# Performance work log

Hardware: AMD Instinct MI355X
Metric: run time of the kernel (lower is better)

The kernel has to match this reference:

```python
import jax, jax.numpy as jnp
import numpy as np

N = 50000
E = 800000
IN_DIM = 128
OUT_DIM = 128
EDGE_DIM = 3
H = 4
HD = OUT_DIM // H  # 32
SCALE = HD ** -0.5


def setup_inputs() -> dict:
    key = jax.random.key(0)
    ks = jax.random.split(key, 10)
    x = jax.random.normal(ks[0], (N, IN_DIM), dtype=jnp.float32)
    edge_index = jax.random.randint(ks[1], (2, E), 0, N, dtype=jnp.int64)
    edge_attr = jax.random.normal(ks[2], (E, EDGE_DIM), dtype=jnp.float32)
    s = 1.0 / np.sqrt(IN_DIM)
    Wq = jax.random.normal(ks[3], (IN_DIM, H * HD), dtype=jnp.float32) * s
    Wk = jax.random.normal(ks[4], (IN_DIM, H * HD), dtype=jnp.float32) * s
    Wv = jax.random.normal(ks[5], (IN_DIM, H * HD), dtype=jnp.float32) * s
    We = jax.random.normal(ks[6], (EDGE_DIM, H), dtype=jnp.float32) * (1.0 / np.sqrt(EDGE_DIM))
    Wo = jax.random.normal(ks[7], (H * HD, OUT_DIM), dtype=jnp.float32) * (1.0 / np.sqrt(H * HD))
    bo = jnp.zeros((OUT_DIM,), dtype=jnp.float32)
    Wm = jax.random.normal(ks[8], (IN_DIM + OUT_DIM, OUT_DIM), dtype=jnp.float32) * (1.0 / np.sqrt(IN_DIM + OUT_DIM))
    bm = jnp.zeros((OUT_DIM,), dtype=jnp.float32)
    return {"x": x, "edge_index": edge_index, "edge_attr": edge_attr,
            "Wq": Wq, "Wk": Wk, "Wv": Wv, "We": We, "Wo": Wo, "bo": bo,
            "Wm": Wm, "bm": bm}


def reference(x, edge_index, edge_attr, Wq, Wk, Wv, We, Wo, bo, Wm, bm):
    n = x.shape[0]
    src = edge_index[0]
    dst = edge_index[1]
    Q = (x @ Wq).reshape(n, H, HD)
    K = (x @ Wk).reshape(n, H, HD)
    V = (x @ Wv).reshape(n, H, HD)
    edge_bias = edge_attr @ We                                  # [E, H]
    attn = jnp.sum(Q[dst] * K[src], axis=-1) * SCALE + edge_bias  # [E, H]
    attn = jnp.where(attn >= 0, attn, 0.2 * attn)               # leaky_relu(0.2)
    # NOTE: original uses a single GLOBAL max over all edges/heads for stability
    attn_exp = jnp.exp(attn - jnp.max(attn))
    attn_sum = jax.ops.segment_sum(attn_exp, dst, num_segments=n)  # [N, H]
    attn_norm = attn_exp / jnp.maximum(attn_sum[dst], 1e-12)
    # dropout disabled (eval mode)
    weighted_V = V[src] * attn_norm[:, :, None]                 # [E, H, HD]
    agg = jax.ops.segment_sum(weighted_V, dst, num_segments=n)  # [N, H, HD]
    agg = agg.reshape(n, H * HD) @ Wo + bo                      # [N, OUT]
    h = jnp.concatenate([x, agg], axis=1) @ Wm + bm
    return jax.nn.relu(h)
```

## Files before the change

kernel.cpp:

```cpp
#include <hip/hip_runtime.h>
#include <hip/hip_bf16.h>
#include <math.h>

#define NN 50000
#define NE 800000
#define DIM 128
#define NH 4
#define HD 32
#define ATTN_SCALE 0.17677669529663687f
#define MTILE 64
#define GEMM_BLOCKS 782
#define NBK 782
#define PTS 2048
#define HBLKS 104

#define K1_QKV_BASE 104
#define K1_WXB_BASE 296
#define K1_GRID     361
#define K3_PART_N     391
#define K3_PACKO_BASE 391
#define K3_XCVT_BASE  519
#define K3_GRID       6769
#define K4_CSR_N 782
#define K4_GRID  1564

typedef unsigned int uint;
typedef unsigned short ushort;
typedef __attribute__((ext_vector_type(8))) short short8;
typedef __attribute__((ext_vector_type(4))) float f32x4;

__device__ inline ushort f2bf(float f) {
    __hip_bfloat16 h = __float2bfloat16(f);
    return *(ushort*)&h;
}
__device__ inline float bflo(uint u) { return __uint_as_float(u << 16); }
__device__ inline float bfhi(uint u) { return __uint_as_float(u & 0xffff0000u); }

__global__ __launch_bounds__(256) void k1_kernel(
    const int* __restrict__ dst, int* __restrict__ bkt_cnt,
    const float* __restrict__ Wq, const float* __restrict__ Wk,
    const float* __restrict__ Wv, short* __restrict__ BpQKV,
    const float* __restrict__ Wo, const float* __restrict__ Wm,
    const float* __restrict__ bo, const float* __restrict__ bm,
    float* __restrict__ Wx, float* __restrict__ bprime)
{
    const int bid = blockIdx.x;
    const int tid = threadIdx.x;

    if (bid < HBLKS) {
        __shared__ int c[NBK];
        for (int l = tid; l < NBK; l += 256) c[l] = 0;
        __syncthreads();
        for (int e = bid * 256 + tid; e < NE; e += HBLKS * 256)
            atomicAdd(&c[dst[e] >> 6], 1);
        __syncthreads();
        for (int l = tid; l < NBK; l += 256)
            if (c[l]) atomicAdd(&bkt_cnt[l], c[l]);
    } else if (bid < K1_WXB_BASE) {
        const int idx = (bid - K1_QKV_BASE) * 256 + tid;
        const int j = idx & 7, lane = (idx >> 3) & 63;
        const int rest = idx >> 9;
        const int nt = rest % 24, kc = rest / 24;
        const int k = kc * 32 + (lane >> 4) * 8 + j;
        const int n = nt * 16 + (lane & 15);
        const float* W = (n < 128) ? Wq : (n < 256 ? Wk : Wv);
        BpQKV[idx] = (short)f2bf(W[k * 128 + (n & 127)]);
    } else {
        const int r = (bid - K1_WXB_BASE) * 2 + (tid >> 7);
        const int j = tid & 127;
        if (r < 128) {
            float acc = 0.f;
            for (int t = 0; t < 128; ++t)
                acc = fmaf(Wo[r * 128 + t], Wm[(128 + t) * 128 + j], acc);
            Wx[r * 128 + j] = acc;
        } else if (r == 128) {
            float acc = bm[j];
            for (int t = 0; t < 128; ++t)
                acc = fmaf(bo[t], Wm[(128 + t) * 128 + j], acc);
            bprime[j] = acc;
        }
    }
}

__global__ __launch_bounds__(256) void bkt_scan_kernel(
    const int* __restrict__ bkt_cnt,
    int* __restrict__ bkt_base, int* __restrict__ bkt_cursor,
    int* __restrict__ rowptr)
{
    __shared__ int part[256];
    const int tid = threadIdx.x;
    const int b0 = tid * 4;
    int v0 = 0, v1 = 0, v2 = 0, v3 = 0;
    if (b0 + 0 < NBK) v0 = bkt_cnt[b0 + 0];
    if (b0 + 1 < NBK) v1 = bkt_cnt[b0 + 1];
    if (b0 + 2 < NBK) v2 = bkt_cnt[b0 + 2];
    if (b0 + 3 < NBK) v3 = bkt_cnt[b0 + 3];
    const int s = v0 + v1 + v2 + v3;
    part[tid] = s;
    __syncthreads();
    for (int off = 1; off < 256; off <<= 1) {
        const int y = (tid >= off) ? part[tid - off] : 0;
        __syncthreads();
        part[tid] += y;
        __syncthreads();
    }
    const int ex = part[tid] - s;
    const int r0 = ex, r1 = ex + v0, r2 = ex + v0 + v1, r3 = ex + v0 + v1 + v2;
    if (b0 + 0 < NBK) { bkt_base[b0 + 0] = r0; bkt_cursor[b0 + 0] = r0; }
    if (b0 + 1 < NBK) { bkt_base[b0 + 1] = r1; bkt_cursor[b0 + 1] = r1; }
    if (b0 + 2 < NBK) { bkt_base[b0 + 2] = r2; bkt_cursor[b0 + 2] = r2; }
    if (b0 + 3 < NBK) { bkt_base[b0 + 3] = r3; bkt_cursor[b0 + 3] = r3; }
    if (tid == 255) bkt_base[NBK] = part[255];
    if (tid == 0)   rowptr[NN] = NE;
}

__global__ __launch_bounds__(256) void k3_kernel(
    const int* __restrict__ src, const int* __restrict__ dst,
    const float* __restrict__ edge_attr, const float* __restrict__ We,
    int* __restrict__ bkt_cursor,
    uint* __restrict__ ppack, uint2* __restrict__ pebp,
    const float* __restrict__ Wm, const float* __restrict__ Wx,
    short* __restrict__ BpOut,
    const float* __restrict__ x, ushort* __restrict__ xb)
{
    const int bid = blockIdx.x;
    const int tid = threadIdx.x;

    if (bid < K3_PART_N) {
        __shared__ int cnt[NBK], rbase[NBK], cnt2[NBK];
        for (int l = tid; l < NBK; l += 256) cnt[l] = 0;
        __syncthreads();
        const int e0 = bid * PTS;
        #pragma unroll
        for (int it = 0; it < 8; ++it) {
            const int e = e0 + it * 256 + tid;
            if (e < NE) atomicAdd(&cnt[dst[e] >> 6], 1);
        }
        __syncthreads();
        for (int l = tid; l < NBK; l += 256) {
            const int c = cnt[l];
            rbase[l] = c ? atomicAdd(&bkt_cursor[l], c) : 0;
            cnt2[l] = 0;
        }
        __syncthreads();
        #pragma unroll
        for (int it = 0; it < 8; ++it) {
            const int e = e0 + it * 256 + tid;
            if (e < NE) {
                const int d = dst[e];
                const int b = d >> 6;
                const int r = atomicAdd(&cnt2[b], 1);
                const int pos = rbase[b] + r;
                ppack[pos] = (uint)src[e] | ((uint)(d & 63) << 16);
                const float a0 = edge_attr[e * 3 + 0];
                const float a1 = edge_attr[e * 3 + 1];
                const float a2 = edge_attr[e * 3 + 2];
                const float b0 = a0 * We[0] + a1 * We[4] + a2 * We[8];
                const float b1 = a0 * We[1] + a1 * We[5] + a2 * We[9];
                const float b2 = a0 * We[2] + a1 * We[6] + a2 * We[10];
                const float b3 = a0 * We[3] + a1 * We[7] + a2 * We[11];
                uint2 ep;
                ep.x = (uint)f2bf(b0) | ((uint)f2bf(b1) << 16);
                ep.y = (uint)f2bf(b2) | ((uint)f2bf(b3) << 16);
                pebp[pos] = ep;
            }
        }
    } else if (bid < K3_XCVT_BASE) {
        const int idx = (bid - K3_PACKO_BASE) * 256 + tid;
        const int j = idx & 7, lane = (idx >> 3) & 63;
        const int rest = idx >> 9;
        const int nt = rest & 7, kc = rest >> 3;
        const int k = kc * 32 + (lane >> 4) * 8 + j;
        const int n = nt * 16 + (lane & 15);
        const float v = (k < 128) ? Wm[k * 128 + n] : Wx[(k - 128) * 128 + n];
        BpOut[idx] = (short)f2bf(v);
    } else {
        const int i = (bid - K3_XCVT_BASE) * 256 + tid;
        const float4 v = ((const float4*)x)[i];
        ushort4 o;
        o.x = f2bf(v.x); o.y = f2bf(v.y); o.z = f2bf(v.z); o.w = f2bf(v.w);
        ((ushort4*)xb)[i] = o;
    }
}

__global__ __launch_bounds__(256) void k4_kernel(
    const int* __restrict__ bkt_base,
    const uint* __restrict__ ppack, const uint2* __restrict__ pebp,
    int* __restrict__ rowptr, uint4* __restrict__ edata,
    const ushort* __restrict__ xb, const short* __restrict__ BpQKV,
    ushort* __restrict__ Qb, ushort* __restrict__ KVb)
{
    const int bid = blockIdx.x;
    const int tid = threadIdx.x;

    if (bid < K4_CSR_N) {
        __shared__ int cnt[64];
        __shared__ int pre[64];
        const int base = bkt_base[bid];
        const int n = bkt_base[bid + 1] - base;
        const int node0 = bid << 6;

        if (tid < 64) cnt[tid] = 0;
        __syncthreads();
        for (int i = base + tid; i < base + n; i += 256)
            atomicAdd(&cnt[ppack[i] >> 16], 1);
        __syncthreads();

        if (tid < 64) {
            const int c = cnt[tid];
            int xsc = c;
            #pragma unroll
            for (int off = 1; off < 64; off <<= 1) {
                const int y = __shfl_up(xsc, off);
                if (tid >= off) xsc += y;
            }
            const int ex = base + xsc - c;
            pre[tid] = ex;
            const int g = node0 + tid;
            if (g < NN) rowptr[g] = ex;
        }
        __syncthreads();

        for (int i = base + tid; i < base + n; i += 256) {
            const uint v = ppack[i];
            const int pos = atomicAdd(&pre[v >> 16], 1);
            const uint2 ep = pebp[i];
            uint4 rec;
            rec.x = v & 0xFFFFu;
            rec.y = ep.x;
            rec.z = ep.y;
            rec.w = 0u;
            edata[pos] = rec;
        }
    } else {
        const int qb = bid - K4_CSR_N;
        const int wave = tid >> 6;
        const int lane = tid & 63;
        const int m = lane & 15, quad = lane >> 4;
        const int row0w = qb * MTILE + wave * 16;
        const int arow = row0w + m;
        const bool rowok = arow < NN;

        short8 a[4];
        #pragma unroll
        for (int kc = 0; kc < 4; ++kc)
            a[kc] = rowok ? *(const short8*)(xb + (size_t)arow * 128 + kc * 32 + quad * 8)
                          : (short8)(0);

        const int NT = 24;
        for (int nt = 0; nt < NT; nt += 2) {
            f32x4 acc0 = {0.f, 0.f, 0.f, 0.f}, acc1 = {0.f, 0.f, 0.f, 0.f};
            #pragma unroll
            for (int kc = 0; kc < 4; ++kc) {
                const short8 b0 = *(const short8*)(BpQKV + ((size_t)(kc * NT + nt) * 64 + lane) * 8);
                const short8 b1 = *(const short8*)(BpQKV + ((size_t)(kc * NT + nt + 1) * 64 + lane) * 8);
                acc0 = __builtin_amdgcn_mfma_f32_16x16x32_bf16(a[kc], b0, acc0, 0, 0, 0);
                acc1 = __builtin_amdgcn_mfma_f32_16x16x32_bf16(a[kc], b1, acc1, 0, 0, 0);
            }
            #pragma unroll
            for (int t = 0; t < 2; ++t) {
                const f32x4 acc = t ? acc1 : acc0;
                const int c = (nt + t) * 16 + m;
                #pragma unroll
                for (int g = 0; g < 4; ++g) {
                    const int r = row0w + quad * 4 + g;
                    if (r < NN) {
                        if (c < 128) Qb[(size_t)r * 128 + c] = f2bf(acc[g]);
                        else        KVb[(size_t)r * 256 + (c - 128)] = f2bf(acc[g]);
                    }
                }
            }
        }
    }
}

__global__ __launch_bounds__(256) void out_mfma_kernel(
    const ushort* __restrict__ xb, const ushort* __restrict__ aggb,
    const short* __restrict__ Bp, const float* __restrict__ bprime,
    float* __restrict__ out)
{
    const int wave = threadIdx.x >> 6;
    const int lane = threadIdx.x & 63;
    const int m = lane & 15, quad = lane >> 4;
    const int row0w = blockIdx.x * MTILE + wave * 16;
    const int arow = row0w + m;
    const bool rowok = arow < NN;

    short8 a[8];
    #pragma unroll
    for (int kc = 0; kc < 4; ++kc)
        a[kc] = rowok ? *(const short8*)(xb + (size_t)arow * 128 + kc * 32 + quad * 8)
                      : (short8)(0);
    #pragma unroll
    for (int kc = 0; kc < 4; ++kc)
        a[4 + kc] = rowok ? *(const short8*)(aggb + (size_t)arow * 128 + kc * 32 + quad * 8)
                          : (short8)(0);

    const int NT = 8;
    for (int nt = 0; nt < NT; nt += 2) {
        f32x4 acc0 = {0.f, 0.f, 0.f, 0.f}, acc1 = {0.f, 0.f, 0.f, 0.f};
        #pragma unroll
        for (int kc = 0; kc < 8; ++kc) {
            const short8 b0 = *(const short8*)(Bp + ((size_t)(kc * NT + nt) * 64 + lane) * 8);
            const short8 b1 = *(const short8*)(Bp + ((size_t)(kc * NT + nt + 1) * 64 + lane) * 8);
            acc0 = __builtin_amdgcn_mfma_f32_16x16x32_bf16(a[kc], b0, acc0, 0, 0, 0);
            acc1 = __builtin_amdgcn_mfma_f32_16x16x32_bf16(a[kc], b1, acc1, 0, 0, 0);
        }
        #pragma unroll
        for (int t = 0; t < 2; ++t) {
            const f32x4 acc = t ? acc1 : acc0;
            const int c = (nt + t) * 16 + m;
            const float bb = bprime[c];
            #pragma unroll
            for (int g = 0; g < 4; ++g) {
                const int r = row0w + quad * 4 + g;
                if (r < NN) out[(size_t)r * 128 + c] = fmaxf(acc[g] + bb, 0.f);
            }
        }
    }
}

__global__ __launch_bounds__(256) void attn_agg_kernel(
    const ushort* __restrict__ Qb, const ushort* __restrict__ KVb,
    const int* __restrict__ rowptr, const uint4* __restrict__ edata,
    ushort* __restrict__ aggb)
{
    const int tid = threadIdx.x;
    const int d = blockIdx.x * 4 + (tid >> 6);
    const int lane = tid & 63;
    const int g = lane >> 4;
    const int t = lane & 15;
    const int h = t >> 2;
    const int begin = rowptr[d];
    const int end   = rowptr[d + 1];

    const uint4 uq = *(const uint4*)(Qb + (size_t)d * DIM + 8 * t);
    const float q0 = bflo(uq.x), q1 = bfhi(uq.x);
    const float q2 = bflo(uq.y), q3 = bfhi(uq.y);
    const float q4 = bflo(uq.z), q5 = bfhi(uq.z);
    const float q6 = bflo(uq.w), q7 = bfhi(uq.w);

    float ss = 0.f;
    float a0 = 0.f, a1 = 0.f, a2 = 0.f, a3 = 0.f;
    float a4 = 0.f, a5 = 0.f, a6 = 0.f, a7 = 0.f;

    if (begin < end) {
        int ec = begin + g;
        if (ec >= end) ec = end - 1;
        uint4 rec = edata[ec];

        for (int p = begin; p < end; p += 4) {
            const bool ok = (p + g) < end;
            const int pn = p + 4;
            uint4 recn = rec;
            if (pn < end) {
                int en = pn + g;
                if (en >= end) en = end - 1;
                recn = edata[en];
            }

            const int s = (int)rec.x;
            const uint wrd = (h & 2) ? rec.z : rec.y;
            const float eb = (h & 1) ? bfhi(wrd) : bflo(wrd);

            const ushort* kv = KVb + (size_t)s * 256 + 8 * t;
            const uint4 uk = *(const uint4*)(kv);
            const uint4 uv = *(const uint4*)(kv + 128);

            float da = q0 * bflo(uk.x);
            float db = q1 * bfhi(uk.x);
            da = fmaf(q2, bflo(uk.y), da);
            db = fmaf(q3, bfhi(uk.y), db);
            da = fmaf(q4, bflo(uk.z), da);
            db = fmaf(q5, bfhi(uk.z), db);
            da = fmaf(q6, bflo(uk.w), da);
            db = fmaf(q7, bfhi(uk.w), db);
            float part = da + db;
            part += __shfl_xor(part, 1);
            part += __shfl_xor(part, 2);

            float a = fmaf(part, ATTN_SCALE, eb);
            a = (a >= 0.f) ? a : 0.2f * a;
            const float w = ok ? __expf(a) : 0.f;

            ss += w;
            a0 = fmaf(w, bflo(uv.x), a0);
            a1 = fmaf(w, bfhi(uv.x), a1);
            a2 = fmaf(w, bflo(uv.y), a2);
            a3 = fmaf(w, bfhi(uv.y), a3);
            a4 = fmaf(w, bflo(uv.z), a4);
            a5 = fmaf(w, bfhi(uv.z), a5);
            a6 = fmaf(w, bflo(uv.w), a6);
            a7 = fmaf(w, bfhi(uv.w), a7);

            rec = recn;
        }
    }

    ss += __shfl_xor(ss, 16);
    ss += __shfl_xor(ss, 32);
    a0 += __shfl_xor(a0, 16); a0 += __shfl_xor(a0, 32);
    a1 += __shfl_xor(a1, 16); a1 += __shfl_xor(a1, 32);
    a2 += __shfl_xor(a2, 16); a2 += __shfl_xor(a2, 32);
    a3 += __shfl_xor(a3, 16); a3 += __shfl_xor(a3, 32);
    a4 += __shfl_xor(a4, 16); a4 += __shfl_xor(a4, 32);
    a5 += __shfl_xor(a5, 16); a5 += __shfl_xor(a5, 32);
    a6 += __shfl_xor(a6, 16); a6 += __shfl_xor(a6, 32);
    a7 += __shfl_xor(a7, 16); a7 += __shfl_xor(a7, 32);

    if (g == 0) {
        const float inv = 1.f / fmaxf(ss, 1e-12f);
        uint4 o;
        o.x = (uint)f2bf(a0 * inv) | ((uint)f2bf(a1 * inv) << 16);
        o.y = (uint)f2bf(a2 * inv) | ((uint)f2bf(a3 * inv) << 16);
        o.z = (uint)f2bf(a4 * inv) | ((uint)f2bf(a5 * inv) << 16);
        o.w = (uint)f2bf(a6 * inv) | ((uint)f2bf(a7 * inv) << 16);
        *(uint4*)(aggb + (size_t)d * DIM + 8 * t) = o;
    }
}

extern "C" void kernel_launch(void* const* d_in, const int* in_sizes, int n_in,
                              void* d_out, int out_size, void* d_ws, size_t ws_size,
                              hipStream_t stream)
{
    const float* x         = (const float*)d_in[0];
    const int*   edge_idx  = (const int*)d_in[1];
    const float* edge_attr = (const float*)d_in[2];
    const float* Wq        = (const float*)d_in[3];
    const float* Wk        = (const float*)d_in[4];
    const float* Wv        = (const float*)d_in[5];
    const float* We        = (const float*)d_in[6];
    const float* Wo        = (const float*)d_in[7];
    const float* bo        = (const float*)d_in[8];
    const float* Wm        = (const float*)d_in[9];
    const float* bm        = (const float*)d_in[10];
    float* out = (float*)d_out;

    const int* src = edge_idx;
    const int* dst = edge_idx + NE;

    ushort* xb   = (ushort*)d_ws;
    ushort* Qb   = xb + (size_t)NN * DIM;
    ushort* KVb  = Qb + (size_t)NN * DIM;
    ushort* aggb = KVb + (size_t)NN * 2 * DIM;
    uint*  ppack = (uint*)(aggb + (size_t)NN * DIM);
    uint2* pebp  = (uint2*)(ppack + NE);
    uint4* edata = (uint4*)(pebp + NE);
    float* Wx    = (float*)(edata + NE);
    float* bprime= Wx + 16384;
    short* BpQKV = (short*)(bprime + 128);
    short* BpOut = BpQKV + 49152;
    int*   rowptr= (int*)(BpOut + 32768);
    int*   bkt_cnt    = rowptr + 50048;
    int*   bkt_base   = bkt_cnt + 800;
    int*   bkt_cursor = bkt_base + 800;

    hipMemsetAsync(bkt_cnt, 0, NBK * sizeof(int), stream);

    k1_kernel<<<K1_GRID, 256, 0, stream>>>(
        dst, bkt_cnt, Wq, Wk, Wv, BpQKV, Wo, Wm, bo, bm, Wx, bprime);

    bkt_scan_kernel<<<1, 256, 0, stream>>>(bkt_cnt, bkt_base, bkt_cursor, rowptr);

    k3_kernel<<<K3_GRID, 256, 0, stream>>>(
        src, dst, edge_attr, We, bkt_cursor, ppack, pebp, Wm, Wx, BpOut, x, xb);

    k4_kernel<<<K4_GRID, 256, 0, stream>>>(
        bkt_base, ppack, pebp, rowptr, edata, xb, BpQKV, Qb, KVb);

    attn_agg_kernel<<<NN / 4, 256, 0, stream>>>(Qb, KVb, rowptr, edata, aggb);

    out_mfma_kernel<<<GEMM_BLOCKS, 256, 0, stream>>>(xb, aggb, BpOut, bprime, out);
}
```

Measured before the change: 245.4 us.

## Fuse attention aggregation with output MFMA GEMM via shared-memory tile

Merges the per-node attention aggregation kernel and the output projection GEMM into one 1024-thread kernel. Each block aggregates 16 nodes (one wave per node) into a shared-memory bf16 tile, then 8 waves each compute one 16-column MFMA output slice. This drops the global aggb write and re-read plus one kernel launch. In exchange it uses large blocks with a block-wide barrier, leaves half the waves idle during the GEMM phase, and has each block reload its own B-matrix slices.

```diff
diff --git a/kernel.cpp b/kernel.cpp
--- a/kernel.cpp
+++ b/kernel.cpp
@@ -9,7 +9,6 @@
 #define HD 32
 #define ATTN_SCALE 0.17677669529663687f
 #define MTILE 64
-#define GEMM_BLOCKS 782
 #define NBK 782
 #define PTS 2048
 #define HBLKS 104
@@ -23,6 +22,7 @@
 #define K3_GRID       6769
 #define K4_CSR_N 782
 #define K4_GRID  1564
+#define AO_GRID 3125
 
 typedef unsigned int uint;
 typedef unsigned short ushort;
@@ -274,148 +274,140 @@
     }
 }
 
-__global__ __launch_bounds__(256) void out_mfma_kernel(
-    const ushort* __restrict__ xb, const ushort* __restrict__ aggb,
-    const short* __restrict__ Bp, const float* __restrict__ bprime,
-    float* __restrict__ out)
-{
-    const int wave = threadIdx.x >> 6;
-    const int lane = threadIdx.x & 63;
-    const int m = lane & 15, quad = lane >> 4;
-    const int row0w = blockIdx.x * MTILE + wave * 16;
-    const int arow = row0w + m;
-    const bool rowok = arow < NN;
-
-    short8 a[8];
-    #pragma unroll
-    for (int kc = 0; kc < 4; ++kc)
-        a[kc] = rowok ? *(const short8*)(xb + (size_t)arow * 128 + kc * 32 + quad * 8)
-                      : (short8)(0);
-    #pragma unroll
-    for (int kc = 0; kc < 4; ++kc)
-        a[4 + kc] = rowok ? *(const short8*)(aggb + (size_t)arow * 128 + kc * 32 + quad * 8)
-                          : (short8)(0);
-
-    const int NT = 8;
-    for (int nt = 0; nt < NT; nt += 2) {
-        f32x4 acc0 = {0.f, 0.f, 0.f, 0.f}, acc1 = {0.f, 0.f, 0.f, 0.f};
-        #pragma unroll
-        for (int kc = 0; kc < 8; ++kc) {
-            const short8 b0 = *(const short8*)(Bp + ((size_t)(kc * NT + nt) * 64 + lane) * 8);
-            const short8 b1 = *(const short8*)(Bp + ((size_t)(kc * NT + nt + 1) * 64 + lane) * 8);
-            acc0 = __builtin_amdgcn_mfma_f32_16x16x32_bf16(a[kc], b0, acc0, 0, 0, 0);
-            acc1 = __builtin_amdgcn_mfma_f32_16x16x32_bf16(a[kc], b1, acc1, 0, 0, 0);
-        }
-        #pragma unroll
-        for (int t = 0; t < 2; ++t) {
-            const f32x4 acc = t ? acc1 : acc0;
-            const int c = (nt + t) * 16 + m;
-            const float bb = bprime[c];
-            #pragma unroll
-            for (int g = 0; g < 4; ++g) {
-                const int r = row0w + quad * 4 + g;
-                if (r < NN) out[(size_t)r * 128 + c] = fmaxf(acc[g] + bb, 0.f);
-            }
-        }
-    }
-}
-
-__global__ __launch_bounds__(256) void attn_agg_kernel(
+__global__ __launch_bounds__(1024) void attn_out_kernel(
     const ushort* __restrict__ Qb, const ushort* __restrict__ KVb,
     const int* __restrict__ rowptr, const uint4* __restrict__ edata,
-    ushort* __restrict__ aggb)
-{
+    const ushort* __restrict__ xb, const short* __restrict__ BpOut,
+    const float* __restrict__ bprime, float* __restrict__ out)
+{
+    __shared__ ushort sagg[16][136];
     const int tid = threadIdx.x;
-    const int d = blockIdx.x * 4 + (tid >> 6);
+    const int wv = tid >> 6;
     const int lane = tid & 63;
-    const int g = lane >> 4;
-    const int t = lane & 15;
-    const int h = t >> 2;
-    const int begin = rowptr[d];
-    const int end   = rowptr[d + 1];
-
-    const uint4 uq = *(const uint4*)(Qb + (size_t)d * DIM + 8 * t);
-    const float q0 = bflo(uq.x), q1 = bfhi(uq.x);
-    const float q2 = bflo(uq.y), q3 = bfhi(uq.y);
-    const float q4 = bflo(uq.z), q5 = bfhi(uq.z);
-    const float q6 = bflo(uq.w), q7 = bfhi(uq.w);
-
-    float ss = 0.f;
-    float a0 = 0.f, a1 = 0.f, a2 = 0.f, a3 = 0.f;
-    float a4 = 0.f, a5 = 0.f, a6 = 0.f, a7 = 0.f;
-
-    if (begin < end) {
-        int ec = begin + g;
-        if (ec >= end) ec = end - 1;
-        uint4 rec = edata[ec];
-
-        for (int p = begin; p < end; p += 4) {
-            const bool ok = (p + g) < end;
-            const int pn = p + 4;
-            uint4 recn = rec;
-            if (pn < end) {
-                int en = pn + g;
-                if (en >= end) en = end - 1;
-                recn = edata[en];
+    const int node0 = blockIdx.x * 16;
+
+    {
+        const int d = node0 + wv;
+        const int g = lane >> 4;
+        const int t = lane & 15;
+        const int h = t >> 2;
+        const int begin = rowptr[d];
+        const int end   = rowptr[d + 1];
+
+        const uint4 uq = *(const uint4*)(Qb + (size_t)d * DIM + 8 * t);
+        const float q0 = bflo(uq.x), q1 = bfhi(uq.x);
+        const float q2 = bflo(uq.y), q3 = bfhi(uq.y);
+        const float q4 = bflo(uq.z), q5 = bfhi(uq.z);
+        const float q6 = bflo(uq.w), q7 = bfhi(uq.w);
+
+        float ss = 0.f;
+        float a0 = 0.f, a1 = 0.f, a2 = 0.f, a3 = 0.f;
+        float a4 = 0.f, a5 = 0.f, a6 = 0.f, a7 = 0.f;
+
+        if (begin < end) {
+            int ec = begin + g;
+            if (ec >= end) ec = end - 1;
+            uint4 rec = edata[ec];
+
+            for (int p = begin; p < end; p += 4) {
+                const bool ok = (p + g) < end;
+                const int pn = p + 4;
+                uint4 recn = rec;
+                if (pn < end) {
+                    int en = pn + g;
+                    if (en >= end) en = end - 1;
+                    recn = edata[en];
+                }
+
+                const int s = (int)rec.x;
+                const uint wrd = (h & 2) ? rec.z : rec.y;
+                const float eb = (h & 1) ? bfhi(wrd) : bflo(wrd);
+
+                const ushort* kv = KVb + (size_t)s * 256 + 8 * t;
+                const uint4 uk = *(const uint4*)(kv);
+                const uint4 uv = *(const uint4*)(kv + 128);
+
+                float da = q0 * bflo(uk.x);
+                float db = q1 * bfhi(uk.x);
+                da = fmaf(q2, bflo(uk.y), da);
+                db = fmaf(q3, bfhi(uk.y), db);
+                da = fmaf(q4, bflo(uk.z), da);
+                db = fmaf(q5, bfhi(uk.z), db);
+                da = fmaf(q6, bflo(uk.w), da);
+                db = fmaf(q7, bfhi(uk.w), db);
+                float part = da + db;
+                part += __shfl_xor(part, 1);
+                part += __shfl_xor(part, 2);
+
+                float a = fmaf(part, ATTN_SCALE, eb);
+                a = (a >= 0.f) ? a : 0.2f * a;
+                const float w = ok ? __expf(a) : 0.f;
+
+                ss += w;
+                a0 = fmaf(w, bflo(uv.x), a0);
+                a1 = fmaf(w, bfhi(uv.x), a1);
+                a2 = fmaf(w, bflo(uv.y), a2);
+                a3 = fmaf(w, bfhi(uv.y), a3);
+                a4 = fmaf(w, bflo(uv.z), a4);
+                a5 = fmaf(w, bfhi(uv.z), a5);
+                a6 = fmaf(w, bflo(uv.w), a6);
+                a7 = fmaf(w, bfhi(uv.w), a7);
+
+                rec = recn;
             }
-
-            const int s = (int)rec.x;
-            const uint wrd = (h & 2) ? rec.z : rec.y;
-            const float eb = (h & 1) ? bfhi(wrd) : bflo(wrd);
-
-            const ushort* kv = KVb + (size_t)s * 256 + 8 * t;
-            const uint4 uk = *(const uint4*)(kv);
-            const uint4 uv = *(const uint4*)(kv + 128);
-
-            float da = q0 * bflo(uk.x);
-            float db = q1 * bfhi(uk.x);
-            da = fmaf(q2, bflo(uk.y), da);
-            db = fmaf(q3, bfhi(uk.y), db);
-            da = fmaf(q4, bflo(uk.z), da);
-            db = fmaf(q5, bfhi(uk.z), db);
-            da = fmaf(q6, bflo(uk.w), da);
-            db = fmaf(q7, bfhi(uk.w), db);
-            float part = da + db;
-            part += __shfl_xor(part, 1);
-            part += __shfl_xor(part, 2);
-
-            float a = fmaf(part, ATTN_SCALE, eb);
-            a = (a >= 0.f) ? a : 0.2f * a;
-            const float w = ok ? __expf(a) : 0.f;
-
-            ss += w;
-            a0 = fmaf(w, bflo(uv.x), a0);
-            a1 = fmaf(w, bfhi(uv.x), a1);
-            a2 = fmaf(w, bflo(uv.y), a2);
-            a3 = fmaf(w, bfhi(uv.y), a3);
-            a4 = fmaf(w, bflo(uv.z), a4);
-            a5 = fmaf(w, bfhi(uv.z), a5);
-            a6 = fmaf(w, bflo(uv.w), a6);
-            a7 = fmaf(w, bfhi(uv.w), a7);
-
-            rec = recn;
-        }
-    }
-
-    ss += __shfl_xor(ss, 16);
-    ss += __shfl_xor(ss, 32);
-    a0 += __shfl_xor(a0, 16); a0 += __shfl_xor(a0, 32);
-    a1 += __shfl_xor(a1, 16); a1 += __shfl_xor(a1, 32);
-    a2 += __shfl_xor(a2, 16); a2 += __shfl_xor(a2, 32);
-    a3 += __shfl_xor(a3, 16); a3 += __shfl_xor(a3, 32);
-    a4 += __shfl_xor(a4, 16); a4 += __shfl_xor(a4, 32);
-    a5 += __shfl_xor(a5, 16); a5 += __shfl_xor(a5, 32);
-    a6 += __shfl_xor(a6, 16); a6 += __shfl_xor(a6, 32);
-    a7 += __shfl_xor(a7, 16); a7 += __shfl_xor(a7, 32);
-
-    if (g == 0) {
-        const float inv = 1.f / fmaxf(ss, 1e-12f);
-        uint4 o;
-        o.x = (uint)f2bf(a0 * inv) | ((uint)f2bf(a1 * inv) << 16);
-        o.y = (uint)f2bf(a2 * inv) | ((uint)f2bf(a3 * inv) << 16);
-        o.z = (uint)f2bf(a4 * inv) | ((uint)f2bf(a5 * inv) << 16);
-        o.w = (uint)f2bf(a6 * inv) | ((uint)f2bf(a7 * inv) << 16);
-        *(uint4*)(aggb + (size_t)d * DIM + 8 * t) = o;
+        }
+
+        ss += __shfl_xor(ss, 16);
+        ss += __shfl_xor(ss, 32);
+        a0 += __shfl_xor(a0, 16); a0 += __shfl_xor(a0, 32);
+        a1 += __shfl_xor(a1, 16); a1 += __shfl_xor(a1, 32);
+        a2 += __shfl_xor(a2, 16); a2 += __shfl_xor(a2, 32);
+        a3 += __shfl_xor(a3, 16); a3 += __shfl_xor(a3, 32);
+        a4 += __shfl_xor(a4, 16); a4 += __shfl_xor(a4, 32);
+        a5 += __shfl_xor(a5, 16); a5 += __shfl_xor(a5, 32);
+        a6 += __shfl_xor(a6, 16); a6 += __shfl_xor(a6, 32);
+        a7 += __shfl_xor(a7, 16); a7 += __shfl_xor(a7, 32);
+
+        if (g == 0) {
+            const float inv = 1.f / fmaxf(ss, 1e-12f);
+            uint4 o;
+            o.x = (uint)f2bf(a0 * inv) | ((uint)f2bf(a1 * inv) << 16);
+            o.y = (uint)f2bf(a2 * inv) | ((uint)f2bf(a3 * inv) << 16);
+            o.z = (uint)f2bf(a4 * inv) | ((uint)f2bf(a5 * inv) << 16);
+            o.w = (uint)f2bf(a6 * inv) | ((uint)f2bf(a7 * inv) << 16);
+            *(uint4*)(&sagg[wv][8 * t]) = o;
+        }
+    }
+
+    __syncthreads();
+
+    if (wv < 8) {
+        const int m = lane & 15, quad = lane >> 4;
+        const int arow = node0 + m;
+
+        short8 a[8];
+        #pragma unroll
+        for (int kc = 0; kc < 4; ++kc)
+            a[kc] = *(const short8*)(xb + (size_t)arow * 128 + kc * 32 + quad * 8);
+        #pragma unroll
+        for (int kc = 0; kc < 4; ++kc)
+            a[4 + kc] = *(const short8*)(&sagg[m][kc * 32 + quad * 8]);
+
+        const int NT = 8;
+        const int nt = wv;
+        f32x4 acc = {0.f, 0.f, 0.f, 0.f};
+        #pragma unroll
+        for (int kc = 0; kc < 8; ++kc) {
+            const short8 b0 = *(const short8*)(BpOut + ((size_t)(kc * NT + nt) * 64 + lane) * 8);
+            acc = __builtin_amdgcn_mfma_f32_16x16x32_bf16(a[kc], b0, acc, 0, 0, 0);
+        }
+        const int c = nt * 16 + m;
+        const float bb = bprime[c];
+        #pragma unroll
+        for (int g2 = 0; g2 < 4; ++g2) {
+            const int r = node0 + quad * 4 + g2;
+            out[(size_t)r * 128 + c] = fmaxf(acc[g2] + bb, 0.f);
+        }
     }
 }
 
@@ -442,8 +434,7 @@
     ushort* xb   = (ushort*)d_ws;
     ushort* Qb   = xb + (size_t)NN * DIM;
     ushort* KVb  = Qb + (size_t)NN * DIM;
-    ushort* aggb = KVb + (size_t)NN * 2 * DIM;
-    uint*  ppack = (uint*)(aggb + (size_t)NN * DIM);
+    uint*  ppack = (uint*)(KVb + (size_t)NN * 2 * DIM);
     uint2* pebp  = (uint2*)(ppack + NE);
     uint4* edata = (uint4*)(pebp + NE);
     float* Wx    = (float*)(edata + NE);
@@ -468,7 +459,6 @@
     k4_kernel<<<K4_GRID, 256, 0, stream>>>(
         bkt_base, ppack, pebp, rowptr, edata, xb, BpQKV, Qb, KVb);
 
-    attn_agg_kernel<<<NN / 4, 256, 0, stream>>>(Qb, KVb, rowptr, edata, aggb);
-
-    out_mfma_kernel<<<GEMM_BLOCKS, 256, 0, stream>>>(xb, aggb, BpOut, bprime, out);
-}
+    attn_out_kernel<<<AO_GRID, 1024, 0, stream>>>(
+        Qb, KVb, rowptr, edata, xb, BpOut, bprime, out);
+}
```

Result: no change. 243.7 us (median of 2 runs) (-0.7%).
